# Performance work log

Hardware: AMD Instinct MI355X
Metric: run time of the kernel (lower is better)

## Reference

```python
import jax, jax.numpy as jnp
import numpy as np

N_NODES = 50000
N_EDGES = 800000
IN_CH = 256
HID = 256
NUM_GRAPHS = 512
LEAKY_SLOPE = 0.01
EPS = 1e-5


def gcn_conv(x, src, dst, W, b):
    # src/dst already include self loops. Symmetric normalization D^-1/2 A_hat D^-1/2.
    deg = jnp.zeros((N_NODES,), x.dtype).at[dst].add(1.0)
    dinv = jax.lax.rsqrt(deg)  # deg >= 1 because of self loops
    norm = dinv[src] * dinv[dst]  # [E+N]
    h = x @ W  # [N, H] dense GEMM
    agg = jnp.zeros((N_NODES, W.shape[1]), x.dtype).at[dst].add(h[src] * norm[:, None])
    return agg + b


def layer_norm(x, w, b):
    mu = jnp.mean(x, axis=-1, keepdims=True)
    var = jnp.mean(jnp.square(x - mu), axis=-1, keepdims=True)
    return (x - mu) * jax.lax.rsqrt(var + EPS) * w + b


def setup_inputs() -> dict:
    key = jax.random.key(0)
    ks = jax.random.split(key, 8)
    x = jax.random.normal(ks[0], (N_NODES, IN_CH), dtype=jnp.float32)
    edge_index = jax.random.randint(ks[1], (2, N_EDGES), 0, N_NODES, dtype=jnp.int64)
    batch = jnp.sort(jax.random.randint(ks[2], (N_NODES,), 0, NUM_GRAPHS, dtype=jnp.int64))
    s1 = (2.0 / IN_CH) ** 0.5
    s2 = (2.0 / HID) ** 0.5
    W1 = jax.random.normal(ks[3], (IN_CH, HID), dtype=jnp.float32) * s1
    b1 = jnp.zeros((HID,), jnp.float32)
    W2 = jax.random.normal(ks[4], (HID, HID), dtype=jnp.float32) * s2
    b2 = jnp.zeros((HID,), jnp.float32)
    ln1_w = jnp.ones((HID,), jnp.float32)
    ln1_b = jnp.zeros((HID,), jnp.float32)
    ln2_w = jnp.ones((HID,), jnp.float32)
    ln2_b = jnp.zeros((HID,), jnp.float32)
    return {"x": x, "edge_index": edge_index, "batch": batch,
            "W1": W1, "b1": b1, "ln1_w": ln1_w, "ln1_b": ln1_b,
            "W2": W2, "b2": b2, "ln2_w": ln2_w, "ln2_b": ln2_b}


def reference(x, edge_index, batch, W1, b1, ln1_w, ln1_b, W2, b2, ln2_w, ln2_b):
    loop = jnp.arange(N_NODES, dtype=edge_index.dtype)
    src = jnp.concatenate([edge_index[0], loop])
    dst = jnp.concatenate([edge_index[1], loop])

    h = gcn_conv(x, src, dst, W1, b1)
    h = layer_norm(h, ln1_w, ln1_b)
    h = jnp.where(h >= 0, h, LEAKY_SLOPE * h)

    h = gcn_conv(h, src, dst, W2, b2)
    h = layer_norm(h, ln2_w, ln2_b)
    h = jnp.where(h >= 0, h, LEAKY_SLOPE * h)

    # global mean pool per graph (dropout is inference no-op)
    sums = jax.ops.segment_sum(h, batch, num_segments=NUM_GRAPHS)
    cnts = jax.ops.segment_sum(jnp.ones((N_NODES,), h.dtype), batch, num_segments=NUM_GRAPHS)
    return sums / jnp.maximum(cnts, 1.0)[:, None]
```

## Files before the change

### kernel.cpp

```cpp
#include <hip/hip_runtime.h>

#define N_NODES 50000
#define N_EDGES 800000
#define CH 256
#define NUM_GRAPHS 512
#define LEAKY 0.01f
#define LN_EPS 1e-5f
#define NBLK ((N_NODES + 255) / 256)

typedef __attribute__((ext_vector_type(4))) float f32x4;
typedef __attribute__((ext_vector_type(8))) short bf16x8;

__device__ __forceinline__ float b2f(unsigned short u) {
    union { unsigned int i; float f; } x; x.i = ((unsigned int)u) << 16; return x.f;
}
__device__ __forceinline__ unsigned short f2b(float f) {
    union { float f; unsigned int i; } x; x.f = f;
    unsigned int r = x.i + 0x7fffu + ((x.i >> 16) & 1u);
    return (unsigned short)(r >> 16);
}

__global__ void zero_ints(int* __restrict__ p, int n) {
    int i = blockIdx.x * blockDim.x + threadIdx.x;
    if (i < n) p[i] = 0;
}

__global__ void count_deg(const int* __restrict__ dst, int* __restrict__ cnt) {
    int e = blockIdx.x * blockDim.x + threadIdx.x;
    if (e < N_EDGES) atomicAdd(&cnt[dst[e]], 1);
}

__global__ __launch_bounds__(256) void block_reduce(const int* __restrict__ cnt,
                                                    int* __restrict__ bsum,
                                                    float* __restrict__ dinv) {
    __shared__ int s[256];
    int tid = threadIdx.x;
    int i = blockIdx.x * 256 + tid;
    int v = (i < N_NODES) ? cnt[i] : 0;
    if (i < N_NODES) dinv[i] = rsqrtf(1.0f + (float)v);
    s[tid] = v;
    __syncthreads();
    #pragma unroll
    for (int off = 128; off > 0; off >>= 1) {
        if (tid < off) s[tid] += s[tid + off];
        __syncthreads();
    }
    if (tid == 0) bsum[blockIdx.x] = s[0];
}

__global__ __launch_bounds__(256) void scan_bsums(int* __restrict__ bsum) {
    __shared__ int s[256];
    int tid = threadIdx.x;
    int v = (tid < NBLK) ? bsum[tid] : 0;
    s[tid] = v;
    __syncthreads();
    #pragma unroll
    for (int off = 1; off < 256; off <<= 1) {
        int t = (tid >= off) ? s[tid - off] : 0;
        __syncthreads();
        s[tid] += t;
        __syncthreads();
    }
    if (tid < NBLK) bsum[tid] = s[tid] - v;
}

__global__ __launch_bounds__(256) void block_scan(const int* __restrict__ cnt,
                                                  const int* __restrict__ bsum,
                                                  int* __restrict__ rowptr) {
    __shared__ int s[256];
    int tid = threadIdx.x;
    int i = blockIdx.x * 256 + tid;
    int v = (i < N_NODES) ? cnt[i] : 0;
    s[tid] = v;
    __syncthreads();
    #pragma unroll
    for (int off = 1; off < 256; off <<= 1) {
        int t = (tid >= off) ? s[tid - off] : 0;
        __syncthreads();
        s[tid] += t;
        __syncthreads();
    }
    if (i < N_NODES) rowptr[i + 1] = bsum[blockIdx.x] + s[tid];
    if (i == 0) rowptr[0] = 0;
}

__global__ void fill_csr(const int* __restrict__ src, const int* __restrict__ dst,
                         const int* __restrict__ rowptr, int* __restrict__ cursor,
                         int* __restrict__ col) {
    int e = blockIdx.x * blockDim.x + threadIdx.x;
    if (e < N_EDGES) {
        int d = dst[e];
        int p = rowptr[d] + atomicAdd(&cursor[d], 1);
        col[p] = src[e];
    }
}

__global__ void cast_f32_bf16(const float* __restrict__ in, unsigned short* __restrict__ out, int n4) {
    int i = blockIdx.x * blockDim.x + threadIdx.x;
    if (i < n4) {
        float4 v = ((const float4*)in)[i];
        ushort4 o = make_ushort4(f2b(v.x), f2b(v.y), f2b(v.z), f2b(v.w));
        ((ushort4*)out)[i] = o;
    }
}

__global__ void transpose_w(const float* __restrict__ W, unsigned short* __restrict__ WT) {
    int k = blockIdx.x;
    int n = threadIdx.x;
    WT[n * CH + k] = f2b(W[k * CH + n]);
}

#define BM 128
#define BN 128
#define BK 64
#define SWZ(row, kb) (((row) * 128 + (kb) * 16) ^ (((row) & 7) << 4))

__global__ __launch_bounds__(256) void gemm_bf16(const unsigned short* __restrict__ A,
                                                 const unsigned short* __restrict__ BT,
                                                 const float* __restrict__ dinv,
                                                 unsigned short* __restrict__ out) {
    __shared__ unsigned short As[BM * BK];
    __shared__ unsigned short Bs[BN * BK];
    const int row0 = blockIdx.x * BM;
    const int col0 = blockIdx.y * BN;
    const int tid = threadIdx.x;
    const int w = tid >> 6, l = tid & 63;
    const int wr = w >> 1, wc = w & 1;
    const int lr = l & 15, lg = l >> 4;

    f32x4 acc[4][4] = {};

    for (int k0 = 0; k0 < CH; k0 += BK) {
        #pragma unroll
        for (int it = 0; it < 4; it++) {
            int cidx = it * 256 + tid;
            int r = cidx >> 3, kb = cidx & 7;
            int grow = row0 + r;
            uint4 va = make_uint4(0u, 0u, 0u, 0u);
            if (grow < N_NODES) va = *(const uint4*)&A[(size_t)grow * CH + k0 + kb * 8];
            *(uint4*)((char*)As + SWZ(r, kb)) = va;
            uint4 vb = *(const uint4*)&BT[(size_t)(col0 + r) * CH + k0 + kb * 8];
            *(uint4*)((char*)Bs + SWZ(r, kb)) = vb;
        }
        __syncthreads();
        #pragma unroll
        for (int ks = 0; ks < 2; ks++) {
            bf16x8 af[4], bfr[4];
            #pragma unroll
            for (int fm = 0; fm < 4; fm++) {
                int r = wr * 64 + fm * 16 + lr;
                af[fm] = *(const bf16x8*)((const char*)As + SWZ(r, ks * 4 + lg));
            }
            #pragma unroll
            for (int fn = 0; fn < 4; fn++) {
                int r = wc * 64 + fn * 16 + lr;
                bfr[fn] = *(const bf16x8*)((const char*)Bs + SWZ(r, ks * 4 + lg));
            }
            #pragma unroll
            for (int fm = 0; fm < 4; fm++)
                #pragma unroll
                for (int fn = 0; fn < 4; fn++)
                    acc[fm][fn] = __builtin_amdgcn_mfma_f32_16x16x32_bf16(af[fm], bfr[fn], acc[fm][fn], 0, 0, 0);
        }
        __syncthreads();
    }
    #pragma unroll
    for (int fm = 0; fm < 4; fm++) {
        #pragma unroll
        for (int r = 0; r < 4; r++) {
            int grow = row0 + wr * 64 + fm * 16 + lg * 4 + r;
            if (grow < N_NODES) {
                float s = dinv[grow];
                #pragma unroll
                for (int fn = 0; fn < 4; fn++) {
                    int gcol = col0 + wc * 64 + fn * 16 + lr;
                    out[(size_t)grow * CH + gcol] = f2b(acc[fm][fn][r] * s);
                }
            }
        }
    }
}

__global__ __launch_bounds__(256) void agg_ln_bf16(const unsigned short* __restrict__ h,
                                                   const int* __restrict__ rowptr,
                                                   const int* __restrict__ col,
                                                   const float* __restrict__ dinv,
                                                   const float* __restrict__ bias,
                                                   const float* __restrict__ lnw,
                                                   const float* __restrict__ lnb,
                                                   unsigned short* __restrict__ out) {
    const int w = threadIdx.x >> 6, lane = threadIdx.x & 63;
    const int d = blockIdx.x * 4 + w;
    if (d >= N_NODES) return;
    const int c4 = lane * 4;

    ushort4 v = *(const ushort4*)&h[(size_t)d * CH + c4];
    float a0 = b2f(v.x), a1 = b2f(v.y), a2 = b2f(v.z), a3 = b2f(v.w);

    const int e0 = rowptr[d], e1 = rowptr[d + 1];
    for (int base = e0; base < e1; base += 64) {
        int nch = e1 - base; if (nch > 64) nch = 64;
        int cidx = (lane < nch) ? col[base + lane] : 0;
        int j = 0;
        for (; j + 4 <= nch; j += 4) {
            int s0 = __shfl(cidx, j);
            int s1 = __shfl(cidx, j + 1);
            int s2 = __shfl(cidx, j + 2);
            int s3 = __shfl(cidx, j + 3);
            ushort4 u0 = *(const ushort4*)&h[(size_t)s0 * CH + c4];
            ushort4 u1 = *(const ushort4*)&h[(size_t)s1 * CH + c4];
            ushort4 u2 = *(const ushort4*)&h[(size_t)s2 * CH + c4];
            ushort4 u3 = *(const ushort4*)&h[(size_t)s3 * CH + c4];
            a0 += b2f(u0.x) + b2f(u1.x) + b2f(u2.x) + b2f(u3.x);
            a1 += b2f(u0.y) + b2f(u1.y) + b2f(u2.y) + b2f(u3.y);
            a2 += b2f(u0.z) + b2f(u1.z) + b2f(u2.z) + b2f(u3.z);
            a3 += b2f(u0.w) + b2f(u1.w) + b2f(u2.w) + b2f(u3.w);
        }
        for (; j < nch; j++) {
            int s = __shfl(cidx, j);
            ushort4 u = *(const ushort4*)&h[(size_t)s * CH + c4];
            a0 += b2f(u.x); a1 += b2f(u.y); a2 += b2f(u.z); a3 += b2f(u.w);
        }
    }
    const float di = dinv[d];
    float4 bb = *(const float4*)&bias[c4];
    a0 = a0 * di + bb.x; a1 = a1 * di + bb.y; a2 = a2 * di + bb.z; a3 = a3 * di + bb.w;

    float s1 = a0 + a1 + a2 + a3;
    float s2 = a0 * a0 + a1 * a1 + a2 * a2 + a3 * a3;
    #pragma unroll
    for (int off = 32; off > 0; off >>= 1) {
        s1 += __shfl_xor(s1, off);
        s2 += __shfl_xor(s2, off);
    }
    const float mu = s1 * (1.0f / CH);
    const float rstd = rsqrtf(s2 * (1.0f / CH) - mu * mu + LN_EPS);
    float4 wv = *(const float4*)&lnw[c4];
    float4 bv = *(const float4*)&lnb[c4];
    float y0 = (a0 - mu) * rstd * wv.x + bv.x;
    float y1 = (a1 - mu) * rstd * wv.y + bv.y;
    float y2 = (a2 - mu) * rstd * wv.z + bv.z;
    float y3 = (a3 - mu) * rstd * wv.w + bv.w;
    y0 = (y0 >= 0.f) ? y0 : LEAKY * y0;
    y1 = (y1 >= 0.f) ? y1 : LEAKY * y1;
    y2 = (y2 >= 0.f) ? y2 : LEAKY * y2;
    y3 = (y3 >= 0.f) ? y3 : LEAKY * y3;
    *(ushort4*)&out[(size_t)d * CH + c4] = make_ushort4(f2b(y0), f2b(y1), f2b(y2), f2b(y3));
}

__global__ __launch_bounds__(256) void pool_mean_bf16(const unsigned short* __restrict__ feat,
                                                      const int* __restrict__ batch,
                                                      float* __restrict__ out) {
    const int g = blockIdx.x;
    const int w = threadIdx.x >> 6, lane = threadIdx.x & 63;
    int lo = 0, hi = N_NODES;
    while (lo < hi) { int mid = (lo + hi) >> 1; if (batch[mid] < g) lo = mid + 1; else hi = mid; }
    const int start = lo;
    hi = N_NODES;
    while (lo < hi) { int mid = (lo + hi) >> 1; if (batch[mid] < g + 1) lo = mid + 1; else hi = mid; }
    const int end = lo;

    float a0 = 0.f, a1 = 0.f, a2 = 0.f, a3 = 0.f;
    for (int n = start + w; n < end; n += 4) {
        ushort4 u = *(const ushort4*)&feat[(size_t)n * CH + lane * 4];
        a0 += b2f(u.x); a1 += b2f(u.y); a2 += b2f(u.z); a3 += b2f(u.w);
    }
    __shared__ float4 red[4][64];
    red[w][lane] = make_float4(a0, a1, a2, a3);
    __syncthreads();
    if (w == 0) {
        float4 t0 = red[0][lane], t1 = red[1][lane], t2 = red[2][lane], t3 = red[3][lane];
        const float inv = (end > start) ? 1.0f / (float)(end - start) : 0.0f;
        float4 o = make_float4((t0.x + t1.x + t2.x + t3.x) * inv,
                               (t0.y + t1.y + t2.y + t3.y) * inv,
                               (t0.z + t1.z + t2.z + t3.z) * inv,
                               (t0.w + t1.w + t2.w + t3.w) * inv);
        *(float4*)&out[(size_t)g * CH + lane * 4] = o;
    }
}

static inline size_t align256(size_t x) { return (x + 255) & ~(size_t)255; }

extern "C" void kernel_launch(void* const* d_in, const int* in_sizes, int n_in,
                              void* d_out, int out_size, void* d_ws, size_t ws_size,
                              hipStream_t stream) {
    const float* x    = (const float*)d_in[0];
    const int*   edge = (const int*)d_in[1];
    const int*   batch= (const int*)d_in[2];
    const float* W1   = (const float*)d_in[3];
    const float* b1   = (const float*)d_in[4];
    const float* ln1w = (const float*)d_in[5];
    const float* ln1b = (const float*)d_in[6];
    const float* W2   = (const float*)d_in[7];
    const float* b2   = (const float*)d_in[8];
    const float* ln2w = (const float*)d_in[9];
    const float* ln2b = (const float*)d_in[10];

    const int* src = edge;
    const int* dst = edge + N_EDGES;

    char* p = (char*)d_ws;
    int* cnt    = (int*)p;  p += align256(N_NODES * 4);
    int* cursor = (int*)p;  p += align256(N_NODES * 4);
    int* rowptr = (int*)p;  p += align256((N_NODES + 1) * 4);
    int* bsum   = (int*)p;  p += align256(NBLK * 4);
    float* dinv = (float*)p; p += align256(N_NODES * 4);
    int* col    = (int*)p;  p += align256(N_EDGES * 4);
    unsigned short* xb  = (unsigned short*)p; p += align256((size_t)N_NODES * CH * 2);
    unsigned short* wt1 = (unsigned short*)p; p += align256(CH * CH * 2);
    unsigned short* wt2 = (unsigned short*)p; p += align256(CH * CH * 2);
    unsigned short* bufA = (unsigned short*)p; p += align256((size_t)N_NODES * CH * 2);
    unsigned short* bufB = (unsigned short*)p;

    const int ztotal = (int)(align256(N_NODES * 4) / 4 + N_NODES);
    zero_ints<<<(ztotal + 255) / 256, 256, 0, stream>>>(cnt, ztotal);
    count_deg<<<(N_EDGES + 255) / 256, 256, 0, stream>>>(dst, cnt);
    block_reduce<<<NBLK, 256, 0, stream>>>(cnt, bsum, dinv);
    scan_bsums<<<1, 256, 0, stream>>>(bsum);
    block_scan<<<NBLK, 256, 0, stream>>>(cnt, bsum, rowptr);
    fill_csr<<<(N_EDGES + 255) / 256, 256, 0, stream>>>(src, dst, rowptr, cursor, col);

    cast_f32_bf16<<<(N_NODES * CH / 4 + 255) / 256, 256, 0, stream>>>(x, xb, N_NODES * CH / 4);
    transpose_w<<<CH, CH, 0, stream>>>(W1, wt1);
    transpose_w<<<CH, CH, 0, stream>>>(W2, wt2);

    dim3 ggrid((N_NODES + BM - 1) / BM, CH / BN);
    gemm_bf16<<<ggrid, 256, 0, stream>>>(xb, wt1, dinv, bufA);
    agg_ln_bf16<<<(N_NODES + 3) / 4, 256, 0, stream>>>(bufA, rowptr, col, dinv, b1, ln1w, ln1b, bufB);
    gemm_bf16<<<ggrid, 256, 0, stream>>>(bufB, wt2, dinv, bufA);
    agg_ln_bf16<<<(N_NODES + 3) / 4, 256, 0, stream>>>(bufA, rowptr, col, dinv, b2, ln2w, ln2b, bufB);
    pool_mean_bf16<<<NUM_GRAPHS, 256, 0, stream>>>(bufB, batch, (float*)d_out);
}
```

Baseline: 299.3 us.

## Fuse fp32-to-bf16 cast into first GEMM, simplify CSR fill, widen gather unroll

The separate cast kernel for x is removed. A new GEMM variant loads fp32 activations and packs them to bf16 while staging tiles into shared memory, which saves a full read and write pass over the 50k×256 input. The CSR build now writes exclusive offsets straight into the cursor array, so fill_csr no longer reads rowptr and the zeroing pass is smaller. The aggregation gather is unrolled to 8 neighbours and uses packed two-wide bf16 conversion, trading more registers for more loads in flight.

```diff
diff --git a/kernel.cpp b/kernel.cpp
--- a/kernel.cpp
+++ b/kernel.cpp
@@ -9,6 +9,7 @@
 #define NBLK ((N_NODES + 255) / 256)
 
 typedef __attribute__((ext_vector_type(4))) float f32x4;
+typedef __attribute__((ext_vector_type(2))) float f32x2;
 typedef __attribute__((ext_vector_type(8))) short bf16x8;
 
 __device__ __forceinline__ float b2f(unsigned short u) {
@@ -18,6 +19,14 @@
     union { float f; unsigned int i; } x; x.f = f;
     unsigned int r = x.i + 0x7fffu + ((x.i >> 16) & 1u);
     return (unsigned short)(r >> 16);
+}
+__device__ __forceinline__ f32x2 b2f2(unsigned int u) {
+    union { unsigned int i; float f; } lo, hi;
+    lo.i = u << 16; hi.i = u & 0xffff0000u;
+    f32x2 r; r.x = lo.f; r.y = hi.f; return r;
+}
+__device__ __forceinline__ unsigned int pack2(float a, float b) {
+    return (unsigned int)f2b(a) | ((unsigned int)f2b(b) << 16);
 }
 
 __global__ void zero_ints(int* __restrict__ p, int n) {
@@ -66,7 +75,8 @@
 
 __global__ __launch_bounds__(256) void block_scan(const int* __restrict__ cnt,
                                                   const int* __restrict__ bsum,
-                                                  int* __restrict__ rowptr) {
+                                                  int* __restrict__ rowptr,
+                                                  int* __restrict__ cursor) {
     __shared__ int s[256];
     int tid = threadIdx.x;
     int i = blockIdx.x * 256 + tid;
@@ -80,27 +90,21 @@
         s[tid] += t;
         __syncthreads();
     }
-    if (i < N_NODES) rowptr[i + 1] = bsum[blockIdx.x] + s[tid];
-    if (i == 0) rowptr[0] = 0;
+    if (i < N_NODES) {
+        int val = bsum[blockIdx.x] + s[tid] - v;
+        rowptr[i] = val;
+        cursor[i] = val;
+        if (i == N_NODES - 1) rowptr[N_NODES] = bsum[blockIdx.x] + s[tid];
+    }
 }
 
 __global__ void fill_csr(const int* __restrict__ src, const int* __restrict__ dst,
-                         const int* __restrict__ rowptr, int* __restrict__ cursor,
-                         int* __restrict__ col) {
+                         int* __restrict__ cursor, int* __restrict__ col) {
     int e = blockIdx.x * blockDim.x + threadIdx.x;
     if (e < N_EDGES) {
         int d = dst[e];
-        int p = rowptr[d] + atomicAdd(&cursor[d], 1);
+        int p = atomicAdd(&cursor[d], 1);
         col[p] = src[e];
-    }
-}
-
-__global__ void cast_f32_bf16(const float* __restrict__ in, unsigned short* __restrict__ out, int n4) {
-    int i = blockIdx.x * blockDim.x + threadIdx.x;
-    if (i < n4) {
-        float4 v = ((const float4*)in)[i];
-        ushort4 o = make_ushort4(f2b(v.x), f2b(v.y), f2b(v.z), f2b(v.w));
-        ((ushort4*)out)[i] = o;
     }
 }
 
@@ -181,6 +185,78 @@
     }
 }
 
+__global__ __launch_bounds__(256) void gemm_f32a(const float* __restrict__ Af,
+                                                 const unsigned short* __restrict__ BT,
+                                                 const float* __restrict__ dinv,
+                                                 unsigned short* __restrict__ out) {
+    __shared__ unsigned short As[BM * BK];
+    __shared__ unsigned short Bs[BN * BK];
+    const int row0 = blockIdx.x * BM;
+    const int col0 = blockIdx.y * BN;
+    const int tid = threadIdx.x;
+    const int w = tid >> 6, l = tid & 63;
+    const int wr = w >> 1, wc = w & 1;
+    const int lr = l & 15, lg = l >> 4;
+
+    f32x4 acc[4][4] = {};
+
+    for (int k0 = 0; k0 < CH; k0 += BK) {
+        #pragma unroll
+        for (int it = 0; it < 4; it++) {
+            int cidx = it * 256 + tid;
+            int r = cidx >> 3, kb = cidx & 7;
+            int grow = row0 + r;
+            uint4 ua = make_uint4(0u, 0u, 0u, 0u);
+            if (grow < N_NODES) {
+                const float* ap = &Af[(size_t)grow * CH + k0 + kb * 8];
+                float4 v0 = *(const float4*)ap;
+                float4 v1 = *(const float4*)(ap + 4);
+                ua = make_uint4(pack2(v0.x, v0.y), pack2(v0.z, v0.w),
+                                pack2(v1.x, v1.y), pack2(v1.z, v1.w));
+            }
+            *(uint4*)((char*)As + SWZ(r, kb)) = ua;
+            uint4 vb = *(const uint4*)&BT[(size_t)(col0 + r) * CH + k0 + kb * 8];
+            *(uint4*)((char*)Bs + SWZ(r, kb)) = vb;
+        }
+        __syncthreads();
+        #pragma unroll
+        for (int ks = 0; ks < 2; ks++) {
+            bf16x8 af[4], bfr[4];
+            #pragma unroll
+            for (int fm = 0; fm < 4; fm++) {
+                int r = wr * 64 + fm * 16 + lr;
+                af[fm] = *(const bf16x8*)((const char*)As + SWZ(r, ks * 4 + lg));
+            }
+            #pragma unroll
+            for (int fn = 0; fn < 4; fn++) {
+                int r = wc * 64 + fn * 16 + lr;
+                bfr[fn] = *(const bf16x8*)((const char*)Bs + SWZ(r, ks * 4 + lg));
+            }
+            #pragma unroll
+            for (int fm = 0; fm < 4; fm++)
+                #pragma unroll
+                for (int fn = 0; fn < 4; fn++)
+                    acc[fm][fn] = __builtin_amdgcn_mfma_f32_16x16x32_bf16(af[fm], bfr[fn], acc[fm][fn], 0, 0, 0);
+        }
+        __syncthreads();
+    }
+    #pragma unroll
+    for (int fm = 0; fm < 4; fm++) {
+        #pragma unroll
+        for (int r = 0; r < 4; r++) {
+            int grow = row0 + wr * 64 + fm * 16 + lg * 4 + r;
+            if (grow < N_NODES) {
+                float s = dinv[grow];
+                #pragma unroll
+                for (int fn = 0; fn < 4; fn++) {
+                    int gcol = col0 + wc * 64 + fn * 16 + lr;
+                    out[(size_t)grow * CH + gcol] = f2b(acc[fm][fn][r] * s);
+                }
+            }
+        }
+    }
+}
+
 __global__ __launch_bounds__(256) void agg_ln_bf16(const unsigned short* __restrict__ h,
                                                    const int* __restrict__ rowptr,
                                                    const int* __restrict__ col,
@@ -193,35 +269,54 @@
     const int d = blockIdx.x * 4 + w;
     if (d >= N_NODES) return;
     const int c4 = lane * 4;
-
-    ushort4 v = *(const ushort4*)&h[(size_t)d * CH + c4];
-    float a0 = b2f(v.x), a1 = b2f(v.y), a2 = b2f(v.z), a3 = b2f(v.w);
+    const uint2* __restrict__ h2 = (const uint2*)h;
+
+    f32x2 acc01, acc23;
+    {
+        uint2 u = h2[(unsigned)(d * 64 + lane)];
+        acc01 = b2f2(u.x); acc23 = b2f2(u.y);
+    }
 
     const int e0 = rowptr[d], e1 = rowptr[d + 1];
     for (int base = e0; base < e1; base += 64) {
         int nch = e1 - base; if (nch > 64) nch = 64;
         int cidx = (lane < nch) ? col[base + lane] : 0;
         int j = 0;
+        for (; j + 8 <= nch; j += 8) {
+            int s0 = __shfl(cidx, j),     s1 = __shfl(cidx, j + 1);
+            int s2 = __shfl(cidx, j + 2), s3 = __shfl(cidx, j + 3);
+            int s4 = __shfl(cidx, j + 4), s5 = __shfl(cidx, j + 5);
+            int s6 = __shfl(cidx, j + 6), s7 = __shfl(cidx, j + 7);
+            uint2 u0 = h2[(unsigned)(s0 * 64 + lane)];
+            uint2 u1 = h2[(unsigned)(s1 * 64 + lane)];
+            uint2 u2 = h2[(unsigned)(s2 * 64 + lane)];
+            uint2 u3 = h2[(unsigned)(s3 * 64 + lane)];
+            uint2 u4 = h2[(unsigned)(s4 * 64 + lane)];
+            uint2 u5 = h2[(unsigned)(s5 * 64 + lane)];
+            uint2 u6 = h2[(unsigned)(s6 * 64 + lane)];
+            uint2 u7 = h2[(unsigned)(s7 * 64 + lane)];
+            acc01 += b2f2(u0.x) + b2f2(u1.x) + b2f2(u2.x) + b2f2(u3.x);
+            acc23 += b2f2(u0.y) + b2f2(u1.y) + b2f2(u2.y) + b2f2(u3.y);
+            acc01 += b2f2(u4.x) + b2f2(u5.x) + b2f2(u6.x) + b2f2(u7.x);
+            acc23 += b2f2(u4.y) + b2f2(u5.y) + b2f2(u6.y) + b2f2(u7.y);
+        }
         for (; j + 4 <= nch; j += 4) {
-            int s0 = __shfl(cidx, j);
-            int s1 = __shfl(cidx, j + 1);
-            int s2 = __shfl(cidx, j + 2);
-            int s3 = __shfl(cidx, j + 3);
-            ushort4 u0 = *(const ushort4*)&h[(size_t)s0 * CH + c4];
-            ushort4 u1 = *(const ushort4*)&h[(size_t)s1 * CH + c4];
-            ushort4 u2 = *(const ushort4*)&h[(size_t)s2 * CH + c4];
-            ushort4 u3 = *(const ushort4*)&h[(size_t)s3 * CH + c4];
-            a0 += b2f(u0.x) + b2f(u1.x) + b2f(u2.x) + b2f(u3.x);
-            a1 += b2f(u0.y) + b2f(u1.y) + b2f(u2.y) + b2f(u3.y);
-            a2 += b2f(u0.z) + b2f(u1.z) + b2f(u2.z) + b2f(u3.z);
-            a3 += b2f(u0.w) + b2f(u1.w) + b2f(u2.w) + b2f(u3.w);
+            int s0 = __shfl(cidx, j),     s1 = __shfl(cidx, j + 1);
+            int s2 = __shfl(cidx, j + 2), s3 = __shfl(cidx, j + 3);
+            uint2 u0 = h2[(unsigned)(s0 * 64 + lane)];
+            uint2 u1 = h2[(unsigned)(s1 * 64 + lane)];
+            uint2 u2 = h2[(unsigned)(s2 * 64 + lane)];
+            uint2 u3 = h2[(unsigned)(s3 * 64 + lane)];
+            acc01 += b2f2(u0.x) + b2f2(u1.x) + b2f2(u2.x) + b2f2(u3.x);
+            acc23 += b2f2(u0.y) + b2f2(u1.y) + b2f2(u2.y) + b2f2(u3.y);
         }
         for (; j < nch; j++) {
             int s = __shfl(cidx, j);
-            ushort4 u = *(const ushort4*)&h[(size_t)s * CH + c4];
-            a0 += b2f(u.x); a1 += b2f(u.y); a2 += b2f(u.z); a3 += b2f(u.w);
-        }
-    }
+            uint2 u = h2[(unsigned)(s * 64 + lane)];
+            acc01 += b2f2(u.x); acc23 += b2f2(u.y);
+        }
+    }
+    float a0 = acc01.x, a1 = acc01.y, a2 = acc23.x, a3 = acc23.y;
     const float di = dinv[d];
     float4 bb = *(const float4*)&bias[c4];
     a0 = a0 * di + bb.x; a1 = a1 * di + bb.y; a2 = a2 * di + bb.z; a3 = a3 * di + bb.w;
@@ -306,26 +401,23 @@
     int* bsum   = (int*)p;  p += align256(NBLK * 4);
     float* dinv = (float*)p; p += align256(N_NODES * 4);
     int* col    = (int*)p;  p += align256(N_EDGES * 4);
-    unsigned short* xb  = (unsigned short*)p; p += align256((size_t)N_NODES * CH * 2);
     unsigned short* wt1 = (unsigned short*)p; p += align256(CH * CH * 2);
     unsigned short* wt2 = (unsigned short*)p; p += align256(CH * CH * 2);
     unsigned short* bufA = (unsigned short*)p; p += align256((size_t)N_NODES * CH * 2);
     unsigned short* bufB = (unsigned short*)p;
 
-    const int ztotal = (int)(align256(N_NODES * 4) / 4 + N_NODES);
-    zero_ints<<<(ztotal + 255) / 256, 256, 0, stream>>>(cnt, ztotal);
+    zero_ints<<<(N_NODES + 255) / 256, 256, 0, stream>>>(cnt, N_NODES);
     count_deg<<<(N_EDGES + 255) / 256, 256, 0, stream>>>(dst, cnt);
     block_reduce<<<NBLK, 256, 0, stream>>>(cnt, bsum, dinv);
     scan_bsums<<<1, 256, 0, stream>>>(bsum);
-    block_scan<<<NBLK, 256, 0, stream>>>(cnt, bsum, rowptr);
-    fill_csr<<<(N_EDGES + 255) / 256, 256, 0, stream>>>(src, dst, rowptr, cursor, col);
-
-    cast_f32_bf16<<<(N_NODES * CH / 4 + 255) / 256, 256, 0, stream>>>(x, xb, N_NODES * CH / 4);
+    block_scan<<<NBLK, 256, 0, stream>>>(cnt, bsum, rowptr, cursor);
+    fill_csr<<<(N_EDGES + 255) / 256, 256, 0, stream>>>(src, dst, cursor, col);
+
     transpose_w<<<CH, CH, 0, stream>>>(W1, wt1);
     transpose_w<<<CH, CH, 0, stream>>>(W2, wt2);
 
     dim3 ggrid((N_NODES + BM - 1) / BM, CH / BN);
-    gemm_bf16<<<ggrid, 256, 0, stream>>>(xb, wt1, dinv, bufA);
+    gemm_f32a<<<ggrid, 256, 0, stream>>>(x, wt1, dinv, bufA);
     agg_ln_bf16<<<(N_NODES + 3) / 4, 256, 0, stream>>>(bufA, rowptr, col, dinv, b1, ln1w, ln1b, bufB);
     gemm_bf16<<<ggrid, 256, 0, stream>>>(bufB, wt2, dinv, bufA);
     agg_ln_bf16<<<(N_NODES + 3) / 4, 256, 0, stream>>>(bufA, rowptr, col, dinv, b2, ln2w, ln2b, bufB);
```

Result: no change. 303.2 us (+1.3%).
